# Performance work log

Hardware: AMD Instinct MI355X
Metric: run time of the kernel (lower is better)

Reference implementation:

```python
import jax, jax.numpy as jnp
import numpy as np

GS_TAU = 1.0
GS_ITERS = 20
EPS = 1e-20


def setup_inputs() -> dict:
    key = jax.random.key(0)
    k1, k2, k3 = jax.random.split(key, 3)
    B, N, D = 32, 1024, 256
    scores = jax.random.normal(k1, (B, N, D), dtype=jnp.float32)
    W = jax.random.normal(k2, (D, 1), dtype=jnp.float32) * (1.0 / np.sqrt(D))
    b = jnp.zeros((1,), dtype=jnp.float32)
    # U ~ Uniform[0,1); gumbel computed inside reference exactly as torch does
    U = jax.random.uniform(k3, (B, N, N), dtype=jnp.float32)
    gumbel_noise = -jnp.log(-jnp.log(U + EPS) + EPS)
    return {"scores": scores, "W": W, "b": b, "gumbel_noise": gumbel_noise}


def reference(scores, W, b, gumbel_noise):
    # score_proj: (B, N, D) @ (D, 1) -> (B, N)
    scalar_scores = (jnp.einsum('bnd,do->bno', scores, W) + b)[..., 0]
    B, N = scalar_scores.shape
    # broadcast scores along dim 2 (expand(-1,-1,N)), add gumbel, divide by tau
    log_alpha = (scalar_scores[:, :, None] + gumbel_noise) / GS_TAU
    # Sinkhorn normalization in log space
    for _ in range(GS_ITERS):
        log_alpha = log_alpha - jax.scipy.special.logsumexp(log_alpha, axis=2, keepdims=True)
        log_alpha = log_alpha - jax.scipy.special.logsumexp(log_alpha, axis=1, keepdims=True)
    return jnp.exp(log_alpha)
```

## Files before the change

kernel.cpp:

```cpp
#include <hip/hip_runtime.h>
#include <hip/hip_fp16.h>
#include <math.h>

#define BB 32
#define NN 1024
#define SHIFT 8.0f


__global__ __launch_bounds__(256) void exp_rowsum(const float* __restrict__ g,
                                                  __half* __restrict__ K,
                                                  float* __restrict__ u) {
    const int wave = threadIdx.x >> 6, lane = threadIdx.x & 63;
    const int row = blockIdx.x * 4 + wave;
    const float4* grow = (const float4*)(g + ((size_t)row << 10));
    uint2* krow = (uint2*)(K + ((size_t)row << 10));
    float s = 0.f;
    #pragma unroll
    for (int k = 0; k < 4; k++) {
        float4 gg = grow[lane + 64 * k];
        float e0 = __expf(gg.x - SHIFT), e1 = __expf(gg.y - SHIFT);
        float e2 = __expf(gg.z - SHIFT), e3 = __expf(gg.w - SHIFT);
        s += (e0 + e1) + (e2 + e3);
        __half2 h0 = __floats2half2_rn(e0, e1);
        __half2 h1 = __floats2half2_rn(e2, e3);
        uint2 pk;
        pk.x = *(unsigned int*)&h0;
        pk.y = *(unsigned int*)&h1;
        krow[lane + 64 * k] = pk;
    }
    #pragma unroll
    for (int off = 32; off; off >>= 1) s += __shfl_xor(s, off);
    if (lane == 0) u[row] = 1.0f / s;
}

__global__ __launch_bounds__(1024) void col_pass(const __half* __restrict__ K,
                                                 const float* __restrict__ u,
                                                 float* __restrict__ v) {
    const int b = blockIdx.x >> 3, tile = blockIdx.x & 7;
    const int tx = threadIdx.x & 63, ty = threadIdx.x >> 6;
    const __half2* Kh = (const __half2*)(K + ((size_t)b << 20)) + tile * 64 + tx;
    const float* ub = u + (b << 10);
    float2 acc[8];
    #pragma unroll
    for (int q = 0; q < 8; q++) { acc[q].x = 0.f; acc[q].y = 0.f; }
    for (int k = 0; k < 64; k += 8) {
        #pragma unroll
        for (int q = 0; q < 8; q++) {
            int i = ((k + q) << 4) + ty;
            float2 f = __half22float2(Kh[(size_t)i << 9]);
            float ui = ub[i];
            acc[q].x = fmaf(f.x, ui, acc[q].x);
            acc[q].y = fmaf(f.y, ui, acc[q].y);
        }
    }
    float2 a = acc[0];
    #pragma unroll
    for (int q = 1; q < 8; q++) { a.x += acc[q].x; a.y += acc[q].y; }
    __shared__ float2 sm[16][64];
    sm[ty][tx] = a;
    __syncthreads();
    for (int h = 8; h >= 1; h >>= 1) {
        if (ty < h) {
            sm[ty][tx].x += sm[ty + h][tx].x;
            sm[ty][tx].y += sm[ty + h][tx].y;
        }
        __syncthreads();
    }
    if (ty == 0) {
        float2 c = sm[0][tx];
        ((float2*)(v + (b << 10)))[tile * 64 + tx] = make_float2(1.0f / c.x, 1.0f / c.y);
    }
}

__global__ __launch_bounds__(256) void row_pass(const __half* __restrict__ K,
                                                const float* __restrict__ v,
                                                float* __restrict__ u) {
    const int wave = threadIdx.x >> 6, lane = threadIdx.x & 63;
    const int row = blockIdx.x * 4 + wave;
    const int b = row >> 10;
    const uint2* krow = (const uint2*)(K + ((size_t)row << 10));
    const float4* vrow = (const float4*)(v + ((size_t)b << 10));
    float s = 0.f;
    #pragma unroll
    for (int k = 0; k < 4; k++) {
        uint2 pk = krow[lane + 64 * k];
        __half2 h0 = *(__half2*)&pk.x, h1 = *(__half2*)&pk.y;
        float2 f0 = __half22float2(h0), f1 = __half22float2(h1);
        float4 vv = vrow[lane + 64 * k];
        s += f0.x * vv.x + f0.y * vv.y + f1.x * vv.z + f1.y * vv.w;
    }
    #pragma unroll
    for (int off = 32; off; off >>= 1) s += __shfl_xor(s, off);
    if (lane == 0) u[row] = 1.0f / s;
}

__global__ __launch_bounds__(256) void fin_pass(const __half* __restrict__ K,
                                                const float* __restrict__ u,
                                                const float* __restrict__ v,
                                                float* __restrict__ out) {
    const size_t idx4 = (size_t)blockIdx.x * 256 + threadIdx.x;
    const size_t base = idx4 << 2;
    const int row = (int)(base >> 10), b = row >> 10;
    const int j4 = ((int)(base & 1023)) >> 2;
    uint2 pk = ((const uint2*)K)[idx4];
    __half2 h0 = *(__half2*)&pk.x, h1 = *(__half2*)&pk.y;
    float2 f0 = __half22float2(h0), f1 = __half22float2(h1);
    float ui = u[row];
    float4 vv = ((const float4*)(v + ((size_t)b << 10)))[j4];
    float4 o;
    o.x = f0.x * ui * vv.x;
    o.y = f0.y * ui * vv.y;
    o.z = f1.x * ui * vv.z;
    o.w = f1.y * ui * vv.w;
    ((float4*)out)[idx4] = o;
}


template<bool USE_V>
__global__ __launch_bounds__(256) void row_step(const float* __restrict__ g,
                                                const float* __restrict__ v,
                                                float* __restrict__ t) {
    const int wave = threadIdx.x >> 6, lane = threadIdx.x & 63;
    const int row = blockIdx.x * 4 + wave;
    const int b = row >> 10;
    const float4* grow = (const float4*)(g + ((size_t)row << 10));
    const float4* vrow = (const float4*)(v + ((size_t)b << 10));
    float x[16];
    #pragma unroll
    for (int k = 0; k < 4; k++) {
        float4 gg = grow[lane + 64 * k];
        if (USE_V) {
            float4 vv = vrow[lane + 64 * k];
            x[4*k+0] = gg.x + vv.x; x[4*k+1] = gg.y + vv.y;
            x[4*k+2] = gg.z + vv.z; x[4*k+3] = gg.w + vv.w;
        } else {
            x[4*k+0] = gg.x; x[4*k+1] = gg.y; x[4*k+2] = gg.z; x[4*k+3] = gg.w;
        }
    }
    float m = -INFINITY;
    #pragma unroll
    for (int k = 0; k < 16; k++) m = fmaxf(m, x[k]);
    #pragma unroll
    for (int off = 32; off; off >>= 1) m = fmaxf(m, __shfl_xor(m, off));
    float s = 0.f;
    #pragma unroll
    for (int k = 0; k < 16; k++) s += __expf(x[k] - m);
    #pragma unroll
    for (int off = 32; off; off >>= 1) s += __shfl_xor(s, off);
    if (lane == 0) t[row] = -(m + __logf(s));
}

__global__ __launch_bounds__(256) void col_step(const float* __restrict__ g,
                                                const float* __restrict__ t,
                                                float* __restrict__ v) {
    const int b = blockIdx.x >> 4, tile = blockIdx.x & 15;
    const int tx = threadIdx.x & 63, ty = threadIdx.x >> 6;
    const int j = tile * 64 + tx;
    const float* gp = g + ((size_t)b << 20) + j;
    const float* tp = t + (b << 10);
    float m = -INFINITY, s = 0.f;
    for (int it = 0; it < 256; it += 8) {
        float xv[8];
        #pragma unroll
        for (int u2 = 0; u2 < 8; u2++) {
            int i = ((it + u2) << 2) + ty;
            xv[u2] = gp[(size_t)i << 10] + tp[i];
        }
        #pragma unroll
        for (int u2 = 0; u2 < 8; u2++) {
            float nm = fmaxf(m, xv[u2]);
            s = s * __expf(m - nm) + __expf(xv[u2] - nm);
            m = nm;
        }
    }
    __shared__ float sm[4][64];
    __shared__ float ss[4][64];
    sm[ty][tx] = m; ss[ty][tx] = s;
    __syncthreads();
    if (ty == 0) {
        float M = sm[0][tx], S = ss[0][tx];
        #pragma unroll
        for (int k = 1; k < 4; k++) {
            float mk = sm[k][tx], sk = ss[k][tx];
            float nm = fmaxf(M, mk);
            S = S * __expf(M - nm) + sk * __expf(mk - nm);
            M = nm;
        }
        v[(b << 10) + j] = -(M + __logf(S));
    }
}

__global__ __launch_bounds__(256) void finalize_k(const float* __restrict__ g,
                                                  const float* __restrict__ t,
                                                  const float* __restrict__ v,
                                                  float* __restrict__ out) {
    const size_t idx4 = (size_t)blockIdx.x * 256 + threadIdx.x;
    const size_t base = idx4 << 2;
    const int row = (int)(base >> 10), b = row >> 10;
    const int j = (int)(base & 1023);
    const float ti = t[row];
    float4 gg = ((const float4*)g)[idx4];
    float4 vv = ((const float4*)(v + ((size_t)b << 10)))[j >> 2];
    float4 o;
    o.x = __expf(gg.x + ti + vv.x);
    o.y = __expf(gg.y + ti + vv.y);
    o.z = __expf(gg.z + ti + vv.z);
    o.w = __expf(gg.w + ti + vv.w);
    ((float4*)out)[idx4] = o;
}

extern "C" void kernel_launch(void* const* d_in, const int* in_sizes, int n_in,
                              void* d_out, int out_size, void* d_ws, size_t ws_size,
                              hipStream_t stream) {
    const float* g = (const float*)d_in[3];
    float* out = (float*)d_out;
    const size_t needVec = 2ull * BB * NN * sizeof(float);
    const size_t needK   = (size_t)BB * NN * NN * sizeof(__half);

    if (ws_size >= needVec + needK) {
        float* u = (float*)d_ws;
        float* v = u + BB * NN;
        __half* K = (__half*)((char*)d_ws + needVec);
        exp_rowsum<<<8192, 256, 0, stream>>>(g, K, u);
        col_pass<<<256, 1024, 0, stream>>>(K, u, v);
        for (int it = 1; it < 20; it++) {
            row_pass<<<8192, 256, 0, stream>>>(K, v, u);
            col_pass<<<256, 1024, 0, stream>>>(K, u, v);
        }
        fin_pass<<<32768, 256, 0, stream>>>(K, u, v, out);
    } else {
        float* t = (float*)d_ws;
        float* v = t + BB * NN;
        row_step<false><<<8192, 256, 0, stream>>>(g, nullptr, t);
        col_step<<<512, 256, 0, stream>>>(g, t, v);
        for (int it = 1; it < 20; it++) {
            row_step<true><<<8192, 256, 0, stream>>>(g, v, t);
            col_step<<<512, 256, 0, stream>>>(g, t, v);
        }
        finalize_k<<<32768, 256, 0, stream>>>(g, t, v, out);
    }
}
```

Before: 721.4 us.

## Fuse Sinkhorn iterations into one persistent kernel holding K in registers

Replaces the multi-launch scheme (exp pass, 20 row/column passes over an fp16 K stored in global memory, and a final pass) with a single persistent kernel. Each 1024-thread block keeps its 128x1024 slice of K as fp16 in registers, computes column partial sums through shared memory, and combines them across the 8 blocks of a batch with global atomics and a spin-wait counter barrier per iteration. This removes repeated K reads from global memory and about 40 kernel launches. In exchange it depends on all 256 blocks being co-resident for the spin barrier, uses heavy register pressure (64 half2 values per thread plus accumulators), and adds a memset of the per-iteration colsum buffers.

Result: slower. 1.181 ms (+63.7%).

```diff
diff --git a/kernel.cpp b/kernel.cpp
--- a/kernel.cpp
+++ b/kernel.cpp
@@ -5,114 +5,120 @@
 #define BB 32
 #define NN 1024
 #define SHIFT 8.0f
-
-
-__global__ __launch_bounds__(256) void exp_rowsum(const float* __restrict__ g,
-                                                  __half* __restrict__ K,
-                                                  float* __restrict__ u) {
-    const int wave = threadIdx.x >> 6, lane = threadIdx.x & 63;
-    const int row = blockIdx.x * 4 + wave;
-    const float4* grow = (const float4*)(g + ((size_t)row << 10));
-    uint2* krow = (uint2*)(K + ((size_t)row << 10));
-    float s = 0.f;
-    #pragma unroll
-    for (int k = 0; k < 4; k++) {
-        float4 gg = grow[lane + 64 * k];
-        float e0 = __expf(gg.x - SHIFT), e1 = __expf(gg.y - SHIFT);
-        float e2 = __expf(gg.z - SHIFT), e3 = __expf(gg.w - SHIFT);
-        s += (e0 + e1) + (e2 + e3);
-        __half2 h0 = __floats2half2_rn(e0, e1);
-        __half2 h1 = __floats2half2_rn(e2, e3);
-        uint2 pk;
-        pk.x = *(unsigned int*)&h0;
-        pk.y = *(unsigned int*)&h1;
-        krow[lane + 64 * k] = pk;
-    }
-    #pragma unroll
-    for (int off = 32; off; off >>= 1) s += __shfl_xor(s, off);
-    if (lane == 0) u[row] = 1.0f / s;
-}
-
-__global__ __launch_bounds__(1024) void col_pass(const __half* __restrict__ K,
-                                                 const float* __restrict__ u,
-                                                 float* __restrict__ v) {
-    const int b = blockIdx.x >> 3, tile = blockIdx.x & 7;
-    const int tx = threadIdx.x & 63, ty = threadIdx.x >> 6;
-    const __half2* Kh = (const __half2*)(K + ((size_t)b << 20)) + tile * 64 + tx;
-    const float* ub = u + (b << 10);
-    float2 acc[8];
-    #pragma unroll
-    for (int q = 0; q < 8; q++) { acc[q].x = 0.f; acc[q].y = 0.f; }
-    for (int k = 0; k < 64; k += 8) {
-        #pragma unroll
-        for (int q = 0; q < 8; q++) {
-            int i = ((k + q) << 4) + ty;
-            float2 f = __half22float2(Kh[(size_t)i << 9]);
-            float ui = ub[i];
-            acc[q].x = fmaf(f.x, ui, acc[q].x);
-            acc[q].y = fmaf(f.y, ui, acc[q].y);
-        }
-    }
-    float2 a = acc[0];
-    #pragma unroll
-    for (int q = 1; q < 8; q++) { a.x += acc[q].x; a.y += acc[q].y; }
-    __shared__ float2 sm[16][64];
-    sm[ty][tx] = a;
-    __syncthreads();
-    for (int h = 8; h >= 1; h >>= 1) {
-        if (ty < h) {
-            sm[ty][tx].x += sm[ty + h][tx].x;
-            sm[ty][tx].y += sm[ty + h][tx].y;
-        }
-        __syncthreads();
-    }
-    if (ty == 0) {
-        float2 c = sm[0][tx];
-        ((float2*)(v + (b << 10)))[tile * 64 + tx] = make_float2(1.0f / c.x, 1.0f / c.y);
-    }
-}
-
-__global__ __launch_bounds__(256) void row_pass(const __half* __restrict__ K,
-                                                const float* __restrict__ v,
-                                                float* __restrict__ u) {
-    const int wave = threadIdx.x >> 6, lane = threadIdx.x & 63;
-    const int row = blockIdx.x * 4 + wave;
-    const int b = row >> 10;
-    const uint2* krow = (const uint2*)(K + ((size_t)row << 10));
-    const float4* vrow = (const float4*)(v + ((size_t)b << 10));
-    float s = 0.f;
-    #pragma unroll
-    for (int k = 0; k < 4; k++) {
-        uint2 pk = krow[lane + 64 * k];
-        __half2 h0 = *(__half2*)&pk.x, h1 = *(__half2*)&pk.y;
-        float2 f0 = __half22float2(h0), f1 = __half22float2(h1);
-        float4 vv = vrow[lane + 64 * k];
-        s += f0.x * vv.x + f0.y * vv.y + f1.x * vv.z + f1.y * vv.w;
-    }
-    #pragma unroll
-    for (int off = 32; off; off >>= 1) s += __shfl_xor(s, off);
-    if (lane == 0) u[row] = 1.0f / s;
-}
-
-__global__ __launch_bounds__(256) void fin_pass(const __half* __restrict__ K,
-                                                const float* __restrict__ u,
-                                                const float* __restrict__ v,
-                                                float* __restrict__ out) {
-    const size_t idx4 = (size_t)blockIdx.x * 256 + threadIdx.x;
-    const size_t base = idx4 << 2;
-    const int row = (int)(base >> 10), b = row >> 10;
-    const int j4 = ((int)(base & 1023)) >> 2;
-    uint2 pk = ((const uint2*)K)[idx4];
-    __half2 h0 = *(__half2*)&pk.x, h1 = *(__half2*)&pk.y;
-    float2 f0 = __half22float2(h0), f1 = __half22float2(h1);
-    float ui = u[row];
-    float4 vv = ((const float4*)(v + ((size_t)b << 10)))[j4];
-    float4 o;
-    o.x = f0.x * ui * vv.x;
-    o.y = f0.y * ui * vv.y;
-    o.z = f1.x * ui * vv.z;
-    o.w = f1.y * ui * vv.w;
-    ((float4*)out)[idx4] = o;
+#define GS_ITERS 20
+
+__global__ __launch_bounds__(1024, 4) void sinkhorn_persist(
+    const float* __restrict__ g, float* __restrict__ out,
+    float* __restrict__ colsum, int* __restrict__ cnt)
+{
+    const int b    = blockIdx.x >> 3;
+    const int blk  = blockIdx.x & 7;
+    const int wave = threadIdx.x >> 6;
+    const int lane = threadIdx.x & 63;
+    const int tid  = threadIdx.x;
+    const int row0 = blk * 128 + wave * 8;
+
+    const float* gb = g + ((size_t)b << 20);
+    float* ob = out + ((size_t)b << 20);
+
+    __shared__ float sm[16][1024];
+
+    __half2 kr[8][8];
+    float u[8];
+    float vr[16];
+
+    #pragma unroll
+    for (int p = 0; p < 8; ++p) {
+        const float2* grow = (const float2*)(gb + (((size_t)(row0 + p)) << 10)) + lane;
+        float s = 0.f;
+        #pragma unroll
+        for (int c = 0; c < 8; ++c) {
+            float2 gg = grow[c * 64];
+            float e0 = __expf(gg.x - SHIFT);
+            float e1 = __expf(gg.y - SHIFT);
+            s += e0 + e1;
+            kr[p][c] = __floats2half2_rn(e0, e1);
+        }
+        #pragma unroll
+        for (int off = 32; off; off >>= 1) s += __shfl_xor(s, off);
+        u[p] = 1.0f / s;
+    }
+
+    #pragma unroll 1
+    for (int it = 0; it < GS_ITERS; ++it) {
+        float cs[16];
+        #pragma unroll
+        for (int c = 0; c < 16; ++c) cs[c] = 0.f;
+        #pragma unroll
+        for (int p = 0; p < 8; ++p) {
+            const float up = u[p];
+            #pragma unroll
+            for (int c = 0; c < 8; ++c) {
+                float2 f = __half22float2(kr[p][c]);
+                cs[2*c]   = fmaf(f.x, up, cs[2*c]);
+                cs[2*c+1] = fmaf(f.y, up, cs[2*c+1]);
+            }
+        }
+        #pragma unroll
+        for (int c = 0; c < 8; ++c)
+            ((float2*)&sm[wave][0])[c * 64 + lane] = make_float2(cs[2*c], cs[2*c+1]);
+        __syncthreads();
+
+        float bp = 0.f;
+        #pragma unroll
+        for (int w = 0; w < 16; ++w) bp += sm[w][tid];
+        float* csit = colsum + (((size_t)(b * GS_ITERS + it)) << 10);
+        atomicAdd(csit + tid, bp);
+        __syncthreads();
+
+        if (tid == 0) {
+            int* c8 = cnt + b * GS_ITERS + it;
+            __hip_atomic_fetch_add(c8, 1, __ATOMIC_ACQ_REL, __HIP_MEMORY_SCOPE_AGENT);
+            int spins = 0;
+            while (__hip_atomic_load(c8, __ATOMIC_ACQUIRE, __HIP_MEMORY_SCOPE_AGENT) < 8) {
+                __builtin_amdgcn_s_sleep(8);
+                if (++spins > (1 << 22)) break;
+            }
+        }
+        __syncthreads();
+
+        float tot = __hip_atomic_load(csit + tid, __ATOMIC_RELAXED, __HIP_MEMORY_SCOPE_AGENT);
+        sm[0][tid] = 1.0f / tot;
+        __syncthreads();
+        #pragma unroll
+        for (int c = 0; c < 8; ++c) {
+            float2 vv = ((const float2*)&sm[0][0])[c * 64 + lane];
+            vr[2*c] = vv.x; vr[2*c+1] = vv.y;
+        }
+
+        if (it < GS_ITERS - 1) {
+            #pragma unroll
+            for (int p = 0; p < 8; ++p) {
+                float s = 0.f;
+                #pragma unroll
+                for (int c = 0; c < 8; ++c) {
+                    float2 f = __half22float2(kr[p][c]);
+                    s = fmaf(f.x, vr[2*c],   s);
+                    s = fmaf(f.y, vr[2*c+1], s);
+                }
+                #pragma unroll
+                for (int off = 32; off; off >>= 1) s += __shfl_xor(s, off);
+                u[p] = 1.0f / s;
+            }
+        }
+        __syncthreads();
+    }
+
+    #pragma unroll
+    for (int p = 0; p < 8; ++p) {
+        float2* orow = (float2*)(ob + (((size_t)(row0 + p)) << 10)) + lane;
+        const float up = u[p];
+        #pragma unroll
+        for (int c = 0; c < 8; ++c) {
+            float2 f = __half22float2(kr[p][c]);
+            orow[c * 64] = make_float2(f.x * up * vr[2*c], f.y * up * vr[2*c+1]);
+        }
+    }
 }
 
 
@@ -214,20 +220,14 @@
                               hipStream_t stream) {
     const float* g = (const float*)d_in[3];
     float* out = (float*)d_out;
-    const size_t needVec = 2ull * BB * NN * sizeof(float);
-    const size_t needK   = (size_t)BB * NN * NN * sizeof(__half);
-
-    if (ws_size >= needVec + needK) {
-        float* u = (float*)d_ws;
-        float* v = u + BB * NN;
-        __half* K = (__half*)((char*)d_ws + needVec);
-        exp_rowsum<<<8192, 256, 0, stream>>>(g, K, u);
-        col_pass<<<256, 1024, 0, stream>>>(K, u, v);
-        for (int it = 1; it < 20; it++) {
-            row_pass<<<8192, 256, 0, stream>>>(K, v, u);
-            col_pass<<<256, 1024, 0, stream>>>(K, u, v);
-        }
-        fin_pass<<<32768, 256, 0, stream>>>(K, u, v, out);
+    const size_t needCS  = (size_t)BB * GS_ITERS * NN * sizeof(float);
+    const size_t needCnt = (size_t)BB * GS_ITERS * sizeof(int);
+
+    if (ws_size >= needCS + needCnt) {
+        float* colsum = (float*)d_ws;
+        int* cnt = (int*)((char*)d_ws + needCS);
+        hipMemsetAsync(d_ws, 0, needCS + needCnt, stream);
+        sinkhorn_persist<<<BB * 8, 1024, 0, stream>>>(g, out, colsum, cnt);
     } else {
         float* t = (float*)d_ws;
         float* v = t + BB * NN;
```
